# Kernel tuning notes

Hardware: AMD Instinct MI355X
Metric: run time of the kernel (lower is better)

The kernel has to match this reference:

```python
import jax, jax.numpy as jnp
import numpy as np

EPS = 1e-5
NUM_HEADS = 16


def activation_quant(x):
    # 8-bit activation quant with straight-through estimator
    scale = 127.0 / jnp.clip(jnp.max(jnp.abs(x), axis=-1, keepdims=True), 1e-5, None)
    y = jnp.clip(jnp.round(x * scale), -128.0, 127.0) / scale
    return x + jax.lax.stop_gradient(y - x)


def weight_quant(w):
    # ternary {-1,0,1} weight quant with STE
    scale = 1.0 / jnp.clip(jnp.mean(jnp.abs(w)), 1e-5, None)
    wq = jnp.clip(jnp.round(w * scale), -1.0, 1.0) / scale
    return w + jax.lax.stop_gradient(wq - w)


def bitlinear(x, w):
    # F.layer_norm(x, x.shape[1:]): normalize over ALL dims except batch, no affine
    axes = tuple(range(1, x.ndim))
    mu = jnp.mean(x, axis=axes, keepdims=True)
    var = jnp.var(x, axis=axes, keepdims=True)
    xn = (x - mu) * jax.lax.rsqrt(var + EPS)
    return jnp.einsum('bnd,od->bno', activation_quant(xn), weight_quant(w))


def layer_norm(x, gamma, beta):
    mu = jnp.mean(x, axis=-1, keepdims=True)
    var = jnp.var(x, axis=-1, keepdims=True)
    return (x - mu) * jax.lax.rsqrt(var + EPS) * gamma + beta


def setup_inputs() -> dict:
    key = jax.random.key(0)
    k0, k1, k2 = jax.random.split(key, 3)
    B, N, D = 2, 2048, 1024
    return {
        't': jnp.zeros((1,), jnp.float32),
        'x': jax.random.normal(k0, (B, N, D), jnp.float32),
        'w_qkv': jax.random.normal(k1, (3 * D, D), jnp.float32) * 0.02,
        'w_out': jax.random.normal(k2, (D, D), jnp.float32) * 0.02,
        'gamma': jnp.ones((D,), jnp.float32),
        'beta': jnp.zeros((D,), jnp.float32),
    }


def reference(t, x, w_qkv, w_out, gamma, beta):
    B, N, D = x.shape
    H = NUM_HEADS
    hd = D // H
    scale = hd ** -0.5
    h = layer_norm(x, gamma, beta)                     # [B,N,D]
    qkv = bitlinear(h, w_qkv).reshape(B, N, 3, H, hd)   # [B,N,3,H,hd]
    qkv = jnp.transpose(qkv, (2, 0, 3, 1, 4))           # [3,B,H,N,hd]
    q, k, v = qkv[0], qkv[1], qkv[2]
    attn = jax.nn.softmax(jnp.einsum('bhnd,bhmd->bhnm', q, k) * scale, axis=-1)
    out = jnp.einsum('bhnm,bhmd->bhnd', attn, v)        # [B,H,N,hd]
    out = jnp.transpose(out, (0, 2, 1, 3)).reshape(B, N, D)
    return bitlinear(out, w_out)
```

## Files before the change

kernel.cpp:

```cpp
#include <hip/hip_runtime.h>
#include <hip/hip_bf16.h>
#include <hip/hip_fp16.h>
#include <math.h>

typedef __hip_bfloat16 bf16;
typedef int   i32x4  __attribute__((ext_vector_type(4)));
typedef float f32x4  __attribute__((ext_vector_type(4)));
typedef float f32x16 __attribute__((ext_vector_type(16)));
typedef short bfx8   __attribute__((ext_vector_type(8)));

#define EPSV 1e-5f
#define NROWS 4096
#define DIM   1024
#define NSEQ  2048

#define GLDS(gp, lp) __builtin_amdgcn_global_load_lds( \
    (const __attribute__((address_space(1))) void*)(gp), \
    (__attribute__((address_space(3))) void*)(lp), 16, 0, 0)

__device__ __forceinline__ float fexp2(float x){ return __builtin_amdgcn_exp2f(x); }

__device__ __forceinline__ float ldv(const void* p, size_t i, int dt){
  if (dt == 0) return ((const float*)p)[i];
  if (dt == 1) return __bfloat162float(((const bf16*)p)[i]);
  return __half2float(((const __half*)p)[i]);
}
__device__ __forceinline__ float b2f(unsigned u){
  return __uint_as_float(u << 16);
}
__device__ __forceinline__ unsigned short f2bu(float f){
  bf16 t = __float2bfloat16(f);
  return *reinterpret_cast<unsigned short*>(&t);
}

__device__ __forceinline__ void detect(const void* c0, const void* c1,
                                       int& dt, const void*& g, const void*& bta){
  unsigned u0 = *(const unsigned*)c0;
  int gfirst = (u0 != 0u) ? 1 : 0;
  g   = gfirst ? c0 : c1;
  bta = gfirst ? c1 : c0;
  unsigned short g0 = *(const unsigned short*)g;
  dt = (g0 == 0x3F80) ? 1 : ((g0 == 0x3C00) ? 2 : 0);
}

__device__ __forceinline__ float blk_sum(float v, float* sm){
  #pragma unroll
  for (int o = 32; o > 0; o >>= 1) v += __shfl_xor(v, o, 64);
  __syncthreads();
  if ((threadIdx.x & 63) == 0) sm[threadIdx.x >> 6] = v;
  __syncthreads();
  return sm[0] + sm[1] + sm[2] + sm[3];
}
__device__ __forceinline__ double blk_sum_d(double v, double* sm){
  #pragma unroll
  for (int o = 32; o > 0; o >>= 1) v += __shfl_xor(v, o, 64);
  __syncthreads();
  if ((threadIdx.x & 63) == 0) sm[threadIdx.x >> 6] = v;
  __syncthreads();
  return sm[0] + sm[1] + sm[2] + sm[3];
}
__device__ __forceinline__ float blk_max(float v, float* sm){
  #pragma unroll
  for (int o = 32; o > 0; o >>= 1) v = fmaxf(v, __shfl_xor(v, o, 64));
  __syncthreads();
  if ((threadIdx.x & 63) == 0) sm[threadIdx.x >> 6] = v;
  __syncthreads();
  return fmaxf(fmaxf(sm[0], sm[1]), fmaxf(sm[2], sm[3]));
}

__global__ __launch_bounds__(256) void ln_abs(const void* __restrict__ x,
                                              const void* __restrict__ c0,
                                              const void* __restrict__ c1,
                                              const void* __restrict__ wq,
                                              const void* __restrict__ wo,
                                              unsigned short* __restrict__ h,
                                              double* __restrict__ lnp,
                                              double* __restrict__ awp1,
                                              double* __restrict__ awp2){
  __shared__ float sm[4];
  __shared__ double smd[4];
  int dt; const void *g, *bta;
  detect(c0, c1, dt, g, bta);
  int tid = threadIdx.x;
  if (blockIdx.x < 4096){
    int row = blockIdx.x;
    float v[4]; float s = 0.f;
    float gmv[4], btv[4];
    if (dt == 0){
      float4 v4 = ((const float4*)x)[(size_t)row*256 + tid];
      v[0]=v4.x; v[1]=v4.y; v[2]=v4.z; v[3]=v4.w;
      float4 gm4 = ((const float4*)g)[tid];
      float4 bt4 = ((const float4*)bta)[tid];
      gmv[0]=gm4.x; gmv[1]=gm4.y; gmv[2]=gm4.z; gmv[3]=gm4.w;
      btv[0]=bt4.x; btv[1]=bt4.y; btv[2]=bt4.z; btv[3]=bt4.w;
    } else {
      size_t base = (size_t)row * DIM;
      #pragma unroll
      for (int i = 0; i < 4; ++i){
        v[i]   = ldv(x, base + 4*tid + i, dt);
        gmv[i] = ldv(g, 4*tid + i, dt);
        btv[i] = ldv(bta, 4*tid + i, dt);
      }
    }
    #pragma unroll
    for (int i = 0; i < 4; ++i) s += v[i];
    s = blk_sum(s, sm);
    float mu = s * (1.f/1024.f);
    float d2 = 0.f;
    #pragma unroll
    for (int i = 0; i < 4; ++i){ float d = v[i] - mu; d2 += d*d; }
    d2 = blk_sum(d2, sm);
    float rs = rsqrtf(d2 * (1.f/1024.f) + EPSV);
    float hv[4];
    #pragma unroll
    for (int i = 0; i < 4; ++i) hv[i] = (v[i]-mu)*rs*gmv[i] + btv[i];
    unsigned p0 = (unsigned)f2bu(hv[0]) | ((unsigned)f2bu(hv[1]) << 16);
    unsigned p1 = (unsigned)f2bu(hv[2]) | ((unsigned)f2bu(hv[3]) << 16);
    ((uint2*)h)[(size_t)row*256 + tid] = make_uint2(p0, p1);
    double hs = 0.0, hq = 0.0;
    #pragma unroll
    for (int i = 0; i < 4; ++i){ hs += (double)hv[i]; hq += (double)hv[i]*(double)hv[i]; }
    hs = blk_sum_d(hs, smd);
    hq = blk_sum_d(hq, smd);
    if (tid == 0){ lnp[2*row] = hs; lnp[2*row + 1] = hq; }
  } else {
    int blk = blockIdx.x - 4096;
    const void* w; int n; int nblk; int bi; double* part;
    if (blk < 512){ w = wq; n = 3*DIM*DIM; nblk = 512; bi = blk;      part = awp1; }
    else          { w = wo; n = DIM*DIM;   nblk = 128; bi = blk - 512; part = awp2; }
    double s = 0.0;
    if (dt == 0){
      const float4* w4 = (const float4*)w;
      int n4 = n >> 2;
      for (int i = bi*256 + tid; i < n4; i += nblk*256){
        float4 v = w4[i];
        s += (double)(fabsf(v.x) + fabsf(v.y)) + (double)(fabsf(v.z) + fabsf(v.w));
      }
    } else {
      for (int i = bi*256 + tid; i < n; i += nblk*256)
        s += (double)fabsf(ldv(w, i, dt));
    }
    s = blk_sum_d(s, smd);
    if (tid == 0) part[bi] = s;
  }
}

__global__ __launch_bounds__(256) void finalize1(float* acc,
                                                 const double* __restrict__ lnp,
                                                 const double* __restrict__ awp1,
                                                 const double* __restrict__ awp2){
  __shared__ double smd[4];
  int tid = threadIdx.x;
  double s0=0, q0=0, s1=0, q1=0, a1=0, a2=0;
  for (int i = tid; i < 2048; i += 256){
    s0 += lnp[2*i];          q0 += lnp[2*i + 1];
    s1 += lnp[2*(i+2048)];   q1 += lnp[2*(i+2048) + 1];
  }
  for (int i = tid; i < 512; i += 256) a1 += awp1[i];
  if (tid < 128) a2 = awp2[tid];
  s0 = blk_sum_d(s0, smd);  q0 = blk_sum_d(q0, smd);
  s1 = blk_sum_d(s1, smd);  q1 = blk_sum_d(q1, smd);
  a1 = blk_sum_d(a1, smd);  a2 = blk_sum_d(a2, smd);
  if (tid == 0){
    const double cnt = 2097152.0;
    double mu0 = s0/cnt, var0 = q0/cnt - mu0*mu0;
    double mu1 = s1/cnt, var1 = q1/cnt - mu1*mu1;
    acc[16] = (float)mu0; acc[17] = (float)(1.0 / sqrt(var0 + 1e-5));
    acc[18] = (float)mu1; acc[19] = (float)(1.0 / sqrt(var1 + 1e-5));
    acc[20] = (float)(1.0 / fmax(a1 / (3.0*1024.0*1024.0), 1e-5));
    acc[21] = (float)(1.0 / fmax(a2 / (1024.0*1024.0), 1e-5));
  }
}

__global__ __launch_bounds__(256) void finalize2(float* acc,
                                                 const double* __restrict__ atp){
  __shared__ double smd[4];
  int tid = threadIdx.x;
  double s0=0, q0=0, s1=0, q1=0;
  for (int i = tid; i < 1024; i += 256){
    s0 += atp[2*i];           q0 += atp[2*i + 1];
    s1 += atp[2*(i+1024)];    q1 += atp[2*(i+1024) + 1];
  }
  s0 = blk_sum_d(s0, smd);  q0 = blk_sum_d(q0, smd);
  s1 = blk_sum_d(s1, smd);  q1 = blk_sum_d(q1, smd);
  if (tid == 0){
    const double cnt = 2097152.0;
    double mu0 = s0/cnt, var0 = q0/cnt - mu0*mu0;
    double mu1 = s1/cnt, var1 = q1/cnt - mu1*mu1;
    acc[22] = (float)mu0; acc[23] = (float)(1.0 / sqrt(var0 + 1e-5));
    acc[24] = (float)mu1; acc[25] = (float)(1.0 / sqrt(var1 + 1e-5));
  }
}

__global__ __launch_bounds__(256) void quant1_w(const unsigned short* __restrict__ buf,
                                                signed char* __restrict__ qout,
                                                float* __restrict__ rscale,
                                                const void* __restrict__ wqv,
                                                const void* __restrict__ wov,
                                                signed char* __restrict__ wqk,
                                                signed char* __restrict__ wqo,
                                                const float* __restrict__ acc,
                                                const void* __restrict__ c0,
                                                const void* __restrict__ c1){
  __shared__ float sm[4];
  int tid = threadIdx.x;
  if (blockIdx.x < 4096){
    int row = blockIdx.x;
    int b = row >> 11;
    float mu = acc[16 + 2*b], rs = acc[17 + 2*b];
    uint2 pk2 = ((const uint2*)buf)[(size_t)row*256 + tid];
    float v[4];
    v[0] = (b2f(pk2.x & 0xffffu) - mu) * rs;
    v[1] = (b2f(pk2.x >> 16)     - mu) * rs;
    v[2] = (b2f(pk2.y & 0xffffu) - mu) * rs;
    v[3] = (b2f(pk2.y >> 16)     - mu) * rs;
    float am = fmaxf(fmaxf(fabsf(v[0]), fabsf(v[1])), fmaxf(fabsf(v[2]), fabsf(v[3])));
    am = blk_max(am, sm);
    am = fmaxf(am, 1e-5f);
    float s127 = 127.f / am;
    unsigned pk = 0;
    #pragma unroll
    for (int i = 0; i < 4; ++i){
      float q = rintf(v[i] * s127);
      q = fminf(fmaxf(q, -128.f), 127.f);
      pk |= ((unsigned)(unsigned char)(signed char)q) << (8*i);
    }
    ((unsigned*)qout)[(size_t)row*256 + tid] = pk;
    if (tid == 0) rscale[row] = am * (1.f/127.f);
  } else {
    int dt; const void *g, *bta;
    detect(c0, c1, dt, g, bta);
    int bi = blockIdx.x - 4096;
    const int NQ4 = 786432;
    const int NT4 = 1048576;
    float s1 = acc[20], s2 = acc[21];
    if (dt == 0){
      for (int i = bi*256 + tid; i < NT4; i += 1024*256){
        int inq = (i < NQ4);
        const float4* src = inq ? (const float4*)wqv : (const float4*)wov;
        unsigned* dst = inq ? (unsigned*)wqk : (unsigned*)wqo;
        int idx = inq ? i : (i - NQ4);
        float scale = inq ? s1 : s2;
        float4 v = src[idx];
        float vv[4] = {v.x, v.y, v.z, v.w};
        unsigned pk = 0;
        #pragma unroll
        for (int j = 0; j < 4; ++j){
          float q = rintf(vv[j] * scale);
          q = fminf(fmaxf(q, -1.f), 1.f);
          pk |= ((unsigned)(unsigned char)(signed char)q) << (8*j);
        }
        dst[idx] = pk;
      }
    } else {
      const int NQ = 3*DIM*DIM, NT = 4*DIM*DIM;
      for (int i = bi*256 + tid; i < NT; i += 1024*256){
        int inq = (i < NQ);
        int idx = inq ? i : (i - NQ);
        float scale = inq ? s1 : s2;
        float q = rintf(ldv(inq ? wqv : wov, idx, dt) * scale);
        q = fminf(fmaxf(q, -1.f), 1.f);
        (inq ? wqk : wqo)[idx] = (signed char)q;
      }
    }
  }
}

__global__ __launch_bounds__(256) void act_quant_i8b(const unsigned short* __restrict__ buf,
                                                     signed char* __restrict__ qout,
                                                     float* __restrict__ rscale,
                                                     const float* __restrict__ acc,
                                                     int statOff){
  __shared__ float sm[4];
  int row = blockIdx.x;
  int b = row >> 11;
  float mu = acc[statOff + 2*b], rs = acc[statOff + 2*b + 1];
  int tid = threadIdx.x;
  uint2 pk2 = ((const uint2*)buf)[(size_t)row*256 + tid];
  float v[4];
  v[0] = (b2f(pk2.x & 0xffffu) - mu) * rs;
  v[1] = (b2f(pk2.x >> 16)     - mu) * rs;
  v[2] = (b2f(pk2.y & 0xffffu) - mu) * rs;
  v[3] = (b2f(pk2.y >> 16)     - mu) * rs;
  float am = fmaxf(fmaxf(fabsf(v[0]), fabsf(v[1])), fmaxf(fabsf(v[2]), fabsf(v[3])));
  am = blk_max(am, sm);
  am = fmaxf(am, 1e-5f);
  float s127 = 127.f / am;
  unsigned pk = 0;
  #pragma unroll
  for (int i = 0; i < 4; ++i){
    float q = rintf(v[i] * s127);
    q = fminf(fmaxf(q, -128.f), 127.f);
    pk |= ((unsigned)(unsigned char)(signed char)q) << (8*i);
  }
  ((unsigned*)qout)[(size_t)row*256 + tid] = pk;
  if (tid == 0) rscale[row] = am * (1.f/127.f);
}

__global__ __launch_bounds__(256) void gemm_i8(const signed char* __restrict__ A,
                                               const signed char* __restrict__ W,
                                               const float* __restrict__ rscale,
                                               const float* __restrict__ acc, int sidx,
                                               float* __restrict__ Cf,
                                               bf16* __restrict__ Cb,
                                               int ldc, int writeBf, float q_prescale){
  __shared__ __attribute__((aligned(16))) signed char Asl[2][128][64];
  __shared__ __attribute__((aligned(16))) signed char Bsl[2][128][64];
  int tid = threadIdx.x, lane = tid & 63, w = tid >> 6;
  int wr = w >> 1, wc = w & 1;
  int l15 = lane & 15, g = lane >> 4;

  int nwgx = gridDim.x;
  int flat = blockIdx.y * nwgx + blockIdx.x;
  int nwg  = nwgx * gridDim.y;
  int cpx  = nwg >> 3;
  int swzb = (flat & 7) * cpx + (flat >> 3);
  int r0 = (swzb / nwgx) * 128, o0 = (swzb % nwgx) * 128;

  i32x4 zz = {0,0,0,0};
  i32x4 accv[4][4];
  #pragma unroll
  for (int m = 0; m < 4; ++m)
    #pragma unroll
    for (int n = 0; n < 4; ++n) accv[m][n] = zz;

  int srow = (w << 4) | (lane >> 2);
  int sws  = ((lane >> 2) ^ (lane >> 4)) & 3;
  int srcb = (((lane & 3) ^ sws) << 4);
  const signed char* gA0 = A + (size_t)(r0 + srow)*1024 + srcb;
  const signed char* gA1 = A + (size_t)(r0 + srow + 64)*1024 + srcb;
  const signed char* gB0 = W + (size_t)(o0 + srow)*1024 + srcb;
  const signed char* gB1 = W + (size_t)(o0 + srow + 64)*1024 + srcb;

  auto GLOADT = [&](int buf, int kq){
    GLDS(gA0 + kq, &Asl[buf][w*16][0]);
    GLDS(gA1 + kq, &Asl[buf][w*16 + 64][0]);
    GLDS(gB0 + kq, &Bsl[buf][w*16][0]);
    GLDS(gB1 + kq, &Bsl[buf][w*16 + 64][0]);
  };

  GLOADT(0, 0);
  __syncthreads();

  int swr = (l15 ^ (l15 >> 2)) & 3;
  int cb  = ((g ^ swr) << 4);

  int cur = 0;
  for (int k0 = 0; k0 < 1024; k0 += 64){
    if (k0 + 64 < 1024) GLOADT(cur ^ 1, k0 + 64);
    i32x4 af[4], bfr[4];
    #pragma unroll
    for (int m = 0; m < 4; ++m)
      af[m] = *(const i32x4*)&Asl[cur][wr*64 + m*16 + l15][cb];
    #pragma unroll
    for (int n = 0; n < 4; ++n)
      bfr[n] = *(const i32x4*)&Bsl[cur][wc*64 + n*16 + l15][cb];
    __builtin_amdgcn_s_setprio(1);
    #pragma unroll
    for (int m = 0; m < 4; ++m)
      #pragma unroll
      for (int n = 0; n < 4; ++n)
        accv[m][n] = __builtin_amdgcn_mfma_i32_16x16x64_i8(af[m], bfr[n], accv[m][n], 0, 0, 0);
    __builtin_amdgcn_s_setprio(0);
    __syncthreads();
    cur ^= 1;
  }

  float wsc = acc[sidx];
  float cs = (o0 < 1024) ? q_prescale : 1.0f;
  float rf[4][4];
  #pragma unroll
  for (int m = 0; m < 4; ++m)
    #pragma unroll
    for (int r = 0; r < 4; ++r)
      rf[m][r] = rscale[r0 + wr*64 + m*16 + ((lane >> 4) << 2) + r] / wsc * cs;

  #pragma unroll
  for (int m = 0; m < 4; ++m)
    #pragma unroll
    for (int n = 0; n < 4; ++n)
      #pragma unroll
      for (int r = 0; r < 4; ++r){
        float val = (float)accv[m][n][r] * rf[m][r];
        size_t row = (size_t)(r0 + wr*64 + m*16 + ((lane >> 4) << 2) + r);
        int col = o0 + wc*64 + n*16 + l15;
        if (writeBf) Cb[row * ldc + col] = __float2bfloat16(val);
        else         Cf[row * ldc + col] = val;
      }
}

__global__ __launch_bounds__(128) void attn_mfma(const bf16* __restrict__ qkv,
                                                 unsigned short* __restrict__ out,
                                                 double* __restrict__ atp){
  __shared__ __attribute__((aligned(16))) unsigned short K_lds[2][64][64];
  __shared__ __attribute__((aligned(16))) unsigned short Vt_lds[2][64][64];

  int tid = threadIdx.x, lane = tid & 63, w = tid >> 6;
  int l31 = lane & 31, hi = lane >> 5;

  int flat = blockIdx.y * 32 + blockIdx.x;
  int slot = flat & 7, idx = flat >> 3;
  int bh = slot * 4 + (idx >> 5);
  int qx = idx & 31;
  int b = bh >> 4, h = bh & 15;
  int n0 = qx * 64;
  const unsigned short* qg = (const unsigned short*)qkv;

  char* kB = (char*)K_lds;
  char* vB = (char*)Vt_lds;

  int qrow = b*NSEQ + n0 + w*32 + l31;
  bfx8 qf[4];
  #pragma unroll
  for (int kk = 0; kk < 4; ++kk)
    qf[kk] = *(const bfx8*)(qg + (size_t)qrow*3072 + h*64 + kk*16 + hi*8);

  float m_run = -INFINITY, l_run = 0.f;
  f32x16 acco[2];
  #pragma unroll
  for (int n = 0; n < 2; ++n)
    #pragma unroll
    for (int r = 0; r < 16; ++r) acco[n][r] = 0.f;

  int krow = tid & 63;
  int r2 = tid & 31, dw = tid >> 5;
  int k7 = krow & 7;
  int q7 = l31 & 7;

  bfx8 kc[4], vv[4];
  auto LOADT = [&](int kt){
    size_t kvb = (size_t)(b*NSEQ + kt*64);
    #pragma unroll
    for (int j = 0; j < 4; ++j)
      kc[j] = *(const bfx8*)(qg + (kvb + krow)*3072 + 1024 + h*64 + (w + 2*j)*8);
    vv[0] = *(const bfx8*)(qg + (kvb + 2*r2    )*3072 + 2048 + h*64 + dw*8);
    vv[1] = *(const bfx8*)(qg + (kvb + 2*r2 + 1)*3072 + 2048 + h*64 + dw*8);
    vv[2] = *(const bfx8*)(qg + (kvb + 2*r2    )*3072 + 2048 + h*64 + (dw+4)*8);
    vv[3] = *(const bfx8*)(qg + (kvb + 2*r2 + 1)*3072 + 2048 + h*64 + (dw+4)*8);
  };
  auto WRITET = [&](int buf){
    int bo = buf * 8192;
    #pragma unroll
    for (int j = 0; j < 4; ++j)
      *(bfx8*)(kB + bo + krow*128 + (((w + 2*j) ^ k7) << 4)) = kc[j];
    #pragma unroll
    for (int u = 0; u < 8; ++u){
      unsigned w0 = (unsigned)(unsigned short)vv[0][u] |
                    ((unsigned)(unsigned short)vv[1][u] << 16);
      unsigned w1 = (unsigned)(unsigned short)vv[2][u] |
                    ((unsigned)(unsigned short)vv[3][u] << 16);
      *(unsigned*)(vB + bo + (dw*8 + u)*128     + ((4*r2) ^ (u << 4))) = w0;
      *(unsigned*)(vB + bo + ((dw+4)*8 + u)*128 + ((4*r2) ^ (u << 4))) = w1;
    }
  };

  LOADT(0);
  WRITET(0);
  __syncthreads();
  LOADT(1);

  int cur = 0;
  for (int kt = 0; kt < NSEQ/64; ++kt){
    if (kt + 1 < NSEQ/64){
      WRITET(cur ^ 1);
      if (kt + 2 < NSEQ/64) LOADT(kt + 2);
    }
    int bo = cur * 8192;

    f32x16 s0, s1;
    #pragma unroll
    for (int r = 0; r < 16; ++r){ s0[r] = 0.f; s1[r] = 0.f; }
    #pragma unroll
    for (int kk = 0; kk < 4; ++kk){
      bfx8 kb0 = *(const bfx8*)(kB + bo + l31*128        + (((2*kk + hi) ^ q7) << 4));
      bfx8 kb1 = *(const bfx8*)(kB + bo + (32 + l31)*128 + (((2*kk + hi) ^ q7) << 4));
      __builtin_amdgcn_s_setprio(1);
      s0 = __builtin_amdgcn_mfma_f32_32x32x16_bf16(kb0, qf[kk], s0, 0, 0, 0);
      s1 = __builtin_amdgcn_mfma_f32_32x32x16_bf16(kb1, qf[kk], s1, 0, 0, 0);
      __builtin_amdgcn_s_setprio(0);
    }

    float pa0 = fmaxf(s0[0], s0[1]),  pa1 = fmaxf(s0[2], s0[3]);
    float pa2 = fmaxf(s0[4], s0[5]),  pa3 = fmaxf(s0[6], s0[7]);
    #pragma unroll
    for (int r = 8; r < 16; r += 4){
      pa0 = fmaxf(pa0, fmaxf(s0[r], s0[r+1]));
      pa1 = fmaxf(pa1, fmaxf(s0[r+2], s0[r+3]));
    }
    #pragma unroll
    for (int r = 0; r < 16; r += 4){
      pa2 = fmaxf(pa2, fmaxf(s1[r], s1[r+1]));
      pa3 = fmaxf(pa3, fmaxf(s1[r+2], s1[r+3]));
    }
    float pm = fmaxf(fmaxf(pa0, pa1), fmaxf(pa2, pa3));
    pm = fmaxf(pm, __shfl_xor(pm, 32, 64));
    if (__any(pm > m_run + 11.5415605f)){
      float mnew = fmaxf(m_run, pm);
      float corr = fexp2(m_run - mnew);
      m_run = mnew;
      l_run *= corr;
      #pragma unroll
      for (int r = 0; r < 16; ++r){
        float ca = __shfl(corr, (r & 3) + 8*(r >> 2) + 4*hi, 64);
        acco[0][r] *= ca; acco[1][r] *= ca;
      }
    }
    float ts = 0.f;
    #pragma unroll
    for (int r = 0; r < 16; ++r){
      s0[r] = fexp2(s0[r] - m_run); ts += s0[r];
      s1[r] = fexp2(s1[r] - m_run); ts += s1[r];
    }
    ts += __shfl_xor(ts, 32, 64);
    l_run += ts;

    #pragma unroll
    for (int kvb2 = 0; kvb2 < 2; ++kvb2){
      const f32x16& s = kvb2 ? s1 : s0;
      #pragma unroll
      for (int kk2 = 0; kk2 < 2; ++kk2){
        int bse = kk2 * 8;
        unsigned wa, wb2, wc, wd;
        asm("v_cvt_pk_bf16_f32 %0, %1, %2" : "=v"(wa)  : "v"(s[bse+0]), "v"(s[bse+1]));
        asm("v_cvt_pk_bf16_f32 %0, %1, %2" : "=v"(wb2) : "v"(s[bse+4]), "v"(s[bse+5]));
        asm("v_cvt_pk_bf16_f32 %0, %1, %2" : "=v"(wc)  : "v"(s[bse+2]), "v"(s[bse+3]));
        asm("v_cvt_pk_bf16_f32 %0, %1, %2" : "=v"(wd)  : "v"(s[bse+6]), "v"(s[bse+7]));
        asm("v_permlane32_swap_b32 %0, %1" : "+v"(wa), "+v"(wb2));
        asm("v_permlane32_swap_b32 %0, %1" : "+v"(wc), "+v"(wd));
        unsigned pw[4] = {wa, wc, wb2, wd};
        bfx8 pfr = *(bfx8*)pw;
        #pragma unroll
        for (int n = 0; n < 2; ++n){
          bfx8 vb = *(const bfx8*)(vB + bo + (n*32 + l31)*128 +
                                   (((kvb2*4 + kk2*2 + hi) ^ q7) << 4));
          __builtin_amdgcn_s_setprio(1);
          acco[n] = __builtin_amdgcn_mfma_f32_32x32x16_bf16(pfr, vb, acco[n], 0, 0, 0);
          __builtin_amdgcn_s_setprio(0);
        }
      }
    }

    __syncthreads();
    cur ^= 1;
  }

  float il = 1.f / l_run;
  float ila[16];
  #pragma unroll
  for (int r = 0; r < 16; ++r)
    ila[r] = __shfl(il, (r & 3) + 8*(r >> 2) + 4*hi, 64);
  double ssum = 0.0, ssq = 0.0;
  #pragma unroll
  for (int n = 0; n < 2; ++n)
    #pragma unroll
    for (int r = 0; r < 16; ++r){
      float o = acco[n][r] * ila[r];
      int orow = b*NSEQ + n0 + w*32 + (r & 3) + 8*(r >> 2) + 4*hi;
      out[(size_t)orow * DIM + h*64 + n*32 + l31] = f2bu(o);
      ssum += (double)o; ssq += (double)o * (double)o;
    }
  #pragma unroll
  for (int o2 = 32; o2 > 0; o2 >>= 1){
    ssum += __shfl_xor(ssum, o2, 64);
    ssq  += __shfl_xor(ssq,  o2, 64);
  }
  if (lane == 0){
    int widx = (bh * 32 + qx) * 2 + w;
    atp[2*widx] = ssum; atp[2*widx + 1] = ssq;
  }
}

extern "C" void kernel_launch(void* const* d_in, const int* in_sizes, int n_in,
                              void* d_out, int out_size, void* d_ws, size_t ws_size,
                              hipStream_t stream) {
  int ix = -1, iwq = -1, iwo = -1, ig0 = -1, ig1 = -1;
  for (int i = 0; i < n_in; ++i){
    int s = in_sizes[i];
    if      (s == 4194304) ix  = i;
    else if (s == 3145728) iwq = i;
    else if (s == 1048576) iwo = i;
    else if (s == 1024){ if (ig0 < 0) ig0 = i; else ig1 = i; }
  }
  if (ix < 0 || iwq < 0 || iwo < 0 || ig0 < 0 || ig1 < 0){ ix=1; iwq=2; iwo=3; ig0=4; ig1=5; }
  const void* x     = d_in[ix];
  const void* w_qkv = d_in[iwq];
  const void* w_out = d_in[iwo];
  const void* g0    = d_in[ig0];
  const void* g1    = d_in[ig1];

  char* ws = (char*)d_ws;
  float*  acc     = (float*)ws;
  float*  rscale1 = (float*)(ws + 12288);
  float*  rscale2 = (float*)(ws + 28672);
  double* lnp     = (double*)(ws + 65536);
  double* awp1    = (double*)(ws + 131072);
  double* awp2    = (double*)(ws + 135168);
  double* atp     = (double*)(ws + 139264);
  unsigned short* h    = (unsigned short*)(ws + (1u<<20));
  signed char*  h_i8   = (signed char*)(ws + (17u<<20));
  signed char*  wqk_i8 = (signed char*)(ws + (21u<<20));
  signed char*  wqo_i8 = (signed char*)(ws + (24u<<20));
  bf16*         qkvb   = (bf16*)       (ws + (25u<<20));
  signed char*  a2_i8  = (signed char*)(ws + (49u<<20));
  unsigned short* aout = h;

  ln_abs<<<4736, 256, 0, stream>>>(x, g0, g1, w_qkv, w_out, h, lnp, awp1, awp2);
  finalize1<<<1, 256, 0, stream>>>(acc, lnp, awp1, awp2);
  quant1_w<<<5120, 256, 0, stream>>>(h, h_i8, rscale1, w_qkv, w_out,
                                     wqk_i8, wqo_i8, acc, g0, g1);
  gemm_i8<<<dim3(24, 32), 256, 0, stream>>>(h_i8, wqk_i8, rscale1, acc, 20,
                                            nullptr, qkvb, 3072, 1, 0.125f * 1.44269504f);
  attn_mfma<<<dim3(32, 32), 128, 0, stream>>>(qkvb, aout, atp);
  finalize2<<<1, 256, 0, stream>>>(acc, atp);
  act_quant_i8b<<<NROWS, 256, 0, stream>>>(aout, a2_i8, rscale2, acc, 22);
  gemm_i8<<<dim3(8, 32), 256, 0, stream>>>(a2_i8, wqo_i8, rscale2, acc, 21,
                                           (float*)d_out, nullptr, 1024, 0, 1.0f);
}
```

Measured before the change: 147.7 us.

## Split attention KV range in two halves with a separate combine kernel

Splits each query tile's 2048-key loop into two 1024-key halves run by separate blocks, doubling the grid to 2048 blocks, and writes unnormalised partial outputs plus running max and sum. A new combine kernel merges the two halves with log-sum-exp weights, writes the final bf16 output and computes the per-block statistics used by layer norm. The attention loop also drops LDS double buffering for a single buffer with two barriers per tile. The goal is better occupancy across CUs, at the cost of an extra kernel launch, extra global traffic for the partials, and less overlap between loads and compute inside the loop.

```diff
diff --git a/kernel.cpp b/kernel.cpp
--- a/kernel.cpp
+++ b/kernel.cpp
@@ -177,9 +177,9 @@
   __shared__ double smd[4];
   int tid = threadIdx.x;
   double s0=0, q0=0, s1=0, q1=0;
-  for (int i = tid; i < 1024; i += 256){
-    s0 += atp[2*i];           q0 += atp[2*i + 1];
-    s1 += atp[2*(i+1024)];    q1 += atp[2*(i+1024) + 1];
+  for (int i = tid; i < 512; i += 256){
+    s0 += atp[2*i];          q0 += atp[2*i + 1];
+    s1 += atp[2*(i+512)];    q1 += atp[2*(i+512) + 1];
   }
   s0 = blk_sum_d(s0, smd);  q0 = blk_sum_d(q0, smd);
   s1 = blk_sum_d(s1, smd);  q1 = blk_sum_d(q1, smd);
@@ -390,18 +390,19 @@
 }
 
 __global__ __launch_bounds__(128) void attn_mfma(const bf16* __restrict__ qkv,
-                                                 unsigned short* __restrict__ out,
-                                                 double* __restrict__ atp){
-  __shared__ __attribute__((aligned(16))) unsigned short K_lds[2][64][64];
-  __shared__ __attribute__((aligned(16))) unsigned short Vt_lds[2][64][64];
+                                                 unsigned short* __restrict__ op,
+                                                 float2* __restrict__ ml){
+  __shared__ __attribute__((aligned(16))) unsigned short K_lds[64][64];
+  __shared__ __attribute__((aligned(16))) unsigned short Vt_lds[64][64];
 
   int tid = threadIdx.x, lane = tid & 63, w = tid >> 6;
   int l31 = lane & 31, hi = lane >> 5;
 
   int flat = blockIdx.y * 32 + blockIdx.x;
   int slot = flat & 7, idx = flat >> 3;
-  int bh = slot * 4 + (idx >> 5);
-  int qx = idx & 31;
+  int bh = slot * 4 + (idx >> 6);
+  int rem = idx & 63;
+  int qx = rem >> 1, half = rem & 1;
   int b = bh >> 4, h = bh & 15;
   int n0 = qx * 64;
   const unsigned short* qg = (const unsigned short*)qkv;
@@ -429,7 +430,7 @@
 
   bfx8 kc[4], vv[4];
   auto LOADT = [&](int kt){
-    size_t kvb = (size_t)(b*NSEQ + kt*64);
+    size_t kvb = (size_t)(b*NSEQ + half*1024 + kt*64);
     #pragma unroll
     for (int j = 0; j < 4; ++j)
       kc[j] = *(const bfx8*)(qg + (kvb + krow)*3072 + 1024 + h*64 + (w + 2*j)*8);
@@ -438,42 +439,36 @@
     vv[2] = *(const bfx8*)(qg + (kvb + 2*r2    )*3072 + 2048 + h*64 + (dw+4)*8);
     vv[3] = *(const bfx8*)(qg + (kvb + 2*r2 + 1)*3072 + 2048 + h*64 + (dw+4)*8);
   };
-  auto WRITET = [&](int buf){
-    int bo = buf * 8192;
+  auto WRITET = [&](){
     #pragma unroll
     for (int j = 0; j < 4; ++j)
-      *(bfx8*)(kB + bo + krow*128 + (((w + 2*j) ^ k7) << 4)) = kc[j];
+      *(bfx8*)(kB + krow*128 + (((w + 2*j) ^ k7) << 4)) = kc[j];
     #pragma unroll
     for (int u = 0; u < 8; ++u){
       unsigned w0 = (unsigned)(unsigned short)vv[0][u] |
                     ((unsigned)(unsigned short)vv[1][u] << 16);
       unsigned w1 = (unsigned)(unsigned short)vv[2][u] |
                     ((unsigned)(unsigned short)vv[3][u] << 16);
-      *(unsigned*)(vB + bo + (dw*8 + u)*128     + ((4*r2) ^ (u << 4))) = w0;
-      *(unsigned*)(vB + bo + ((dw+4)*8 + u)*128 + ((4*r2) ^ (u << 4))) = w1;
+      *(unsigned*)(vB + (dw*8 + u)*128     + ((4*r2) ^ (u << 4))) = w0;
+      *(unsigned*)(vB + ((dw+4)*8 + u)*128 + ((4*r2) ^ (u << 4))) = w1;
     }
   };
 
   LOADT(0);
-  WRITET(0);
-  __syncthreads();
-  LOADT(1);
-
-  int cur = 0;
-  for (int kt = 0; kt < NSEQ/64; ++kt){
-    if (kt + 1 < NSEQ/64){
-      WRITET(cur ^ 1);
-      if (kt + 2 < NSEQ/64) LOADT(kt + 2);
-    }
-    int bo = cur * 8192;
+
+  for (int kt = 0; kt < 16; ++kt){
+    __syncthreads();
+    WRITET();
+    __syncthreads();
+    if (kt + 1 < 16) LOADT(kt + 1);
 
     f32x16 s0, s1;
     #pragma unroll
     for (int r = 0; r < 16; ++r){ s0[r] = 0.f; s1[r] = 0.f; }
     #pragma unroll
     for (int kk = 0; kk < 4; ++kk){
-      bfx8 kb0 = *(const bfx8*)(kB + bo + l31*128        + (((2*kk + hi) ^ q7) << 4));
-      bfx8 kb1 = *(const bfx8*)(kB + bo + (32 + l31)*128 + (((2*kk + hi) ^ q7) << 4));
+      bfx8 kb0 = *(const bfx8*)(kB + l31*128        + (((2*kk + hi) ^ q7) << 4));
+      bfx8 kb1 = *(const bfx8*)(kB + (32 + l31)*128 + (((2*kk + hi) ^ q7) << 4));
       __builtin_amdgcn_s_setprio(1);
       s0 = __builtin_amdgcn_mfma_f32_32x32x16_bf16(kb0, qf[kk], s0, 0, 0, 0);
       s1 = __builtin_amdgcn_mfma_f32_32x32x16_bf16(kb1, qf[kk], s1, 0, 0, 0);
@@ -531,7 +526,7 @@
         bfx8 pfr = *(bfx8*)pw;
         #pragma unroll
         for (int n = 0; n < 2; ++n){
-          bfx8 vb = *(const bfx8*)(vB + bo + (n*32 + l31)*128 +
+          bfx8 vb = *(const bfx8*)(vB + (n*32 + l31)*128 +
                                    (((kvb2*4 + kk2*2 + hi) ^ q7) << 4));
           __builtin_amdgcn_s_setprio(1);
           acco[n] = __builtin_amdgcn_mfma_f32_32x32x16_bf16(pfr, vb, acco[n], 0, 0, 0);
@@ -539,35 +534,60 @@
         }
       }
     }
-
-    __syncthreads();
-    cur ^= 1;
-  }
-
-  float il = 1.f / l_run;
-  float ila[16];
-  #pragma unroll
-  for (int r = 0; r < 16; ++r)
-    ila[r] = __shfl(il, (r & 3) + 8*(r >> 2) + 4*hi, 64);
+  }
+
+  int rowbase = b*NSEQ + n0 + w*32;
+  #pragma unroll
+  for (int n = 0; n < 2; ++n)
+    #pragma unroll
+    for (int r = 0; r < 16; ++r){
+      int crow = (r & 3) + 8*(r >> 2) + 4*hi;
+      size_t rh = (size_t)(rowbase + crow)*16 + h;
+      op[rh*128 + half*64 + n*32 + l31] = f2bu(acco[n][r]);
+    }
+  if (hi == 0){
+    size_t rh = (size_t)(rowbase + l31)*16 + h;
+    ml[rh*2 + half] = make_float2(m_run, l_run);
+  }
+}
+
+__global__ __launch_bounds__(256) void combine_attn(const unsigned short* __restrict__ op,
+                                                    const float2* __restrict__ ml,
+                                                    unsigned short* __restrict__ aout,
+                                                    double* __restrict__ atp){
+  __shared__ double smd[4];
+  int tid = threadIdx.x;
+  size_t rh = (size_t)blockIdx.x*64 + (tid >> 2);
+  int d0 = (tid & 3) * 16;
+  const unsigned short* base = op + rh*128;
+  bfx8 a0 = *(const bfx8*)(base + d0);
+  bfx8 a1 = *(const bfx8*)(base + d0 + 8);
+  bfx8 bb0 = *(const bfx8*)(base + 64 + d0);
+  bfx8 bb1 = *(const bfx8*)(base + 64 + d0 + 8);
+  float2 m0 = ml[rh*2], m1 = ml[rh*2 + 1];
+  float m = fmaxf(m0.x, m1.x);
+  float c0 = fexp2(m0.x - m), c1 = fexp2(m1.x - m);
+  float inv = 1.f / (m0.y*c0 + m1.y*c1);
+  c0 *= inv; c1 *= inv;
+  float ov[16];
+  #pragma unroll
+  for (int j = 0; j < 8; ++j){
+    ov[j]   = b2f((unsigned short)a0[j])*c0 + b2f((unsigned short)bb0[j])*c1;
+    ov[j+8] = b2f((unsigned short)a1[j])*c0 + b2f((unsigned short)bb1[j])*c1;
+  }
+  unsigned pk[8];
+  #pragma unroll
+  for (int j = 0; j < 8; ++j)
+    pk[j] = (unsigned)f2bu(ov[2*j]) | ((unsigned)f2bu(ov[2*j+1]) << 16);
+  unsigned short* dst = aout + (rh >> 4)*1024 + (rh & 15)*64 + d0;
+  ((uint4*)dst)[0] = make_uint4(pk[0], pk[1], pk[2], pk[3]);
+  ((uint4*)dst)[1] = make_uint4(pk[4], pk[5], pk[6], pk[7]);
   double ssum = 0.0, ssq = 0.0;
   #pragma unroll
-  for (int n = 0; n < 2; ++n)
-    #pragma unroll
-    for (int r = 0; r < 16; ++r){
-      float o = acco[n][r] * ila[r];
-      int orow = b*NSEQ + n0 + w*32 + (r & 3) + 8*(r >> 2) + 4*hi;
-      out[(size_t)orow * DIM + h*64 + n*32 + l31] = f2bu(o);
-      ssum += (double)o; ssq += (double)o * (double)o;
-    }
-  #pragma unroll
-  for (int o2 = 32; o2 > 0; o2 >>= 1){
-    ssum += __shfl_xor(ssum, o2, 64);
-    ssq  += __shfl_xor(ssq,  o2, 64);
-  }
-  if (lane == 0){
-    int widx = (bh * 32 + qx) * 2 + w;
-    atp[2*widx] = ssum; atp[2*widx + 1] = ssq;
-  }
+  for (int j = 0; j < 16; ++j){ ssum += (double)ov[j]; ssq += (double)ov[j]*(double)ov[j]; }
+  ssum = blk_sum_d(ssum, smd);
+  ssq  = blk_sum_d(ssq, smd);
+  if (tid == 0){ atp[2*blockIdx.x] = ssum; atp[2*blockIdx.x + 1] = ssq; }
 }
 
 extern "C" void kernel_launch(void* const* d_in, const int* in_sizes, int n_in,
@@ -596,12 +616,14 @@
   double* awp1    = (double*)(ws + 131072);
   double* awp2    = (double*)(ws + 135168);
   double* atp     = (double*)(ws + 139264);
-  unsigned short* h    = (unsigned short*)(ws + (1u<<20));
+  unsigned short* h     = (unsigned short*)(ws + (1u<<20));
+  unsigned short* opart = (unsigned short*)(ws + (9u<<20));
   signed char*  h_i8   = (signed char*)(ws + (17u<<20));
   signed char*  wqk_i8 = (signed char*)(ws + (21u<<20));
-  signed char*  wqo_i8 = (signed char*)(ws + (24u<<20));
   bf16*         qkvb   = (bf16*)       (ws + (25u<<20));
   signed char*  a2_i8  = (signed char*)(ws + (49u<<20));
+  signed char*  wqo_i8 = (signed char*)(ws + (53u<<20));
+  float2*       mlbuf  = (float2*)     (ws + (54u<<20));
   unsigned short* aout = h;
 
   ln_abs<<<4736, 256, 0, stream>>>(x, g0, g1, w_qkv, w_out, h, lnp, awp1, awp2);
@@ -610,7 +632,8 @@
                                      wqk_i8, wqo_i8, acc, g0, g1);
   gemm_i8<<<dim3(24, 32), 256, 0, stream>>>(h_i8, wqk_i8, rscale1, acc, 20,
                                             nullptr, qkvb, 3072, 1, 0.125f * 1.44269504f);
-  attn_mfma<<<dim3(32, 32), 128, 0, stream>>>(qkvb, aout, atp);
+  attn_mfma<<<dim3(32, 64), 128, 0, stream>>>(qkvb, opart, mlbuf);
+  combine_attn<<<1024, 256, 0, stream>>>(opart, mlbuf, aout, atp);
   finalize2<<<1, 256, 0, stream>>>(acc, atp);
   act_quant_i8b<<<NROWS, 256, 0, stream>>>(aout, a2_i8, rscale2, acc, 22);
   gemm_i8<<<dim3(8, 32), 256, 0, stream>>>(a2_i8, wqo_i8, rscale2, acc, 21,
```

Result: slower. 164.2 us (+11.2%).
